# Performance work log

Measured on AMD Instinct MI355X. Metric: run time of the kernel, lower is better.

Reference implementation:

```python
import jax, jax.numpy as jnp
import numpy as np
from jax import lax

V, E, H, L, T, B = 50000, 512, 1024, 2, 512, 64


def _lstm_layer(x_seq, h0, c0, W_ih, W_hh):
    # x_seq: [T, B, D_in]; W_ih: [4H, D_in]; W_hh: [4H, H]
    x_proj = jnp.einsum('tbd,gd->tbg', x_seq, W_ih)  # precompute input projection

    def step(carry, xp):
        h, c = carry
        gates = xp + h @ W_hh.T  # [B, 4H], PyTorch gate order i,f,g,o
        i, f, g, o = jnp.split(gates, 4, axis=-1)
        i = jax.nn.sigmoid(i)
        f = jax.nn.sigmoid(f)
        g = jnp.tanh(g)
        o = jax.nn.sigmoid(o)
        c = f * c + i * g
        h = o * jnp.tanh(c)
        return (h, c), h

    (hT, cT), ys = lax.scan(step, (h0, c0), x_proj)
    return ys, hT, cT


def setup_inputs() -> dict:
    key = jax.random.key(0)
    ks = jax.random.split(key, 8)
    inputs = jax.random.randint(ks[0], (T, B), 0, V)
    h0 = jnp.zeros((L, B, H), jnp.float32)
    c0 = jnp.zeros((L, B, H), jnp.float32)
    emb = jax.random.uniform(ks[1], (V, E), jnp.float32, -0.1, 0.1)
    s_ih0 = 1.0 / np.sqrt(H)
    W_ih0 = jax.random.uniform(ks[2], (4 * H, E), jnp.float32, -s_ih0, s_ih0)
    W_hh0 = jax.random.uniform(ks[3], (4 * H, H), jnp.float32, -s_ih0, s_ih0)
    W_ih1 = jax.random.uniform(ks[4], (4 * H, H), jnp.float32, -s_ih0, s_ih0)
    W_hh1 = jax.random.uniform(ks[5], (4 * H, H), jnp.float32, -s_ih0, s_ih0)
    dec_W = jax.random.uniform(ks[6], (1, H), jnp.float32, -0.1, 0.1)
    dec_b = jnp.zeros((1,), jnp.float32)
    return {"inputs": inputs, "h0": h0, "c0": c0, "emb": emb,
            "W_ih0": W_ih0, "W_hh0": W_hh0, "W_ih1": W_ih1, "W_hh1": W_hh1,
            "dec_W": dec_W, "dec_b": dec_b}


def reference(inputs, h0, c0, emb, W_ih0, W_hh0, W_ih1, W_hh1, dec_W, dec_b):
    x = emb[inputs]                                      # [T, B, E]
    y0, h1, c1 = _lstm_layer(x, h0[0], c0[0], W_ih0, W_hh0)   # [T, B, H]
    # dropout between layers is inference-disabled (eval mode)
    y1, h2, c2 = _lstm_layer(y0, h0[1], c0[1], W_ih1, W_hh1)  # [T, B, H]
    pooled = jnp.mean(y1, axis=0)                        # [B, H] (squeeze is a no-op)
    decoded = pooled @ dec_W.T + dec_b                   # [B, 1]
    hn = jnp.stack([h1, h2])
    cn = jnp.stack([c1, c2])
    return decoded, hn, cn
```

## Files before the change

kernel.cpp:

```cpp
#include <hip/hip_runtime.h>

#define TT 512
#define BB 64
#define HH 1024
#define EE 512
#define VV 50000
#define BBHH (BB*HH)
#define BPL 128
#define NBLK 256

typedef __attribute__((ext_vector_type(8))) short bf16x8;
typedef __attribute__((ext_vector_type(4))) float f32x4;

__device__ inline unsigned short f2b(float f){
  unsigned int u; __builtin_memcpy(&u, &f, 4);
  unsigned int r = (u + 0x7FFFu + ((u >> 16) & 1u)) >> 16;
  return (unsigned short)r;
}
__device__ inline float sigmoidf_(float x){ return 1.0f / (1.0f + __expf(-x)); }
__device__ inline float tanhf_(float x){ float e = __expf(2.0f * x); return 1.0f - 2.0f / (e + 1.0f); }

__device__ inline bf16x8 pack8(float4 a, float4 b){
  bf16x8 r;
  r[0] = (short)f2b(a.x); r[1] = (short)f2b(a.y); r[2] = (short)f2b(a.z); r[3] = (short)f2b(a.w);
  r[4] = (short)f2b(b.x); r[5] = (short)f2b(b.y); r[6] = (short)f2b(b.z); r[7] = (short)f2b(b.w);
  return r;
}

__global__ void cast_f2b(const float* __restrict__ src, unsigned short* __restrict__ dst, long n){
  long i = ((long)blockIdx.x * blockDim.x + threadIdx.x) * 4;
  long stride = (long)gridDim.x * blockDim.x * 4;
  for (; i + 3 < n; i += stride){
    float4 v = *reinterpret_cast<const float4*>(src + i);
    ushort4 r;
    r.x = f2b(v.x); r.y = f2b(v.y); r.z = f2b(v.z); r.w = f2b(v.w);
    *reinterpret_cast<ushort4*>(dst + i) = r;
  }
}

__global__ void init_h(const float* __restrict__ h0,
                       unsigned short* __restrict__ h0ic, unsigned short* __restrict__ h1ic){
  int i = blockIdx.x * blockDim.x + threadIdx.x;
  int b = i >> 10, j = i & (HH - 1);
  int d = (((j >> 3) * BB) + b) * 8 + (j & 7);
  h0ic[d] = f2b(h0[i]);
  h1ic[d] = f2b(h0[BBHH + i]);
}

__device__ __forceinline__ void wait_layer(const unsigned* __restrict__ f, unsigned e, int lane){
  unsigned a = __hip_atomic_load(f + lane,      __ATOMIC_RELAXED, __HIP_MEMORY_SCOPE_AGENT);
  unsigned b = __hip_atomic_load(f + 64 + lane, __ATOMIC_RELAXED, __HIP_MEMORY_SCOPE_AGENT);
  while (!__all(a >= e && b >= e)){
    __builtin_amdgcn_s_sleep(8);
    a = __hip_atomic_load(f + lane,      __ATOMIC_RELAXED, __HIP_MEMORY_SCOPE_AGENT);
    b = __hip_atomic_load(f + 64 + lane, __ATOMIC_RELAXED, __HIP_MEMORY_SCOPE_AGENT);
  }
}

__device__ __forceinline__ void publish(unsigned* __restrict__ f, int bid_l, unsigned e){
  asm volatile("s_waitcnt vmcnt(0)" ::: "memory");
  __syncthreads();
  if (threadIdx.x == 0)
    __hip_atomic_store(f + bid_l, e, __ATOMIC_RELAXED, __HIP_MEMORY_SCOPE_AGENT);
}

#define LIDX(m, s) ((((m) * 16 + (s)) * 64 + lane) * 4)

#define CBASE ((wid * 32 + hi) * (BB * 8) + l16 * 8)

__device__ void run_l0(
    int bid_l, int lane, int wid, int l16, int hi, int kq,
    const int* __restrict__ inputs, const float* __restrict__ c0,
    const unsigned short* __restrict__ emb_bf,
    const float* __restrict__ Wih0, const float* __restrict__ Whh0,
    const unsigned short* __restrict__ h0ic,
    unsigned short* __restrict__ hist0,
    float* __restrict__ hn, float* __restrict__ cn,
    unsigned* __restrict__ flags0, float* lds)
{
  const int j0 = bid_l * 8;
  const int bown = wid * 16 + l16;
  const int cbase = CBASE;

  bf16x8 wx[2][4], wh[2][8];
  #pragma unroll
  for (int m = 0; m < 2; ++m){
    const int g = l16 & 3;
    const int u = 2 * (l16 >> 2) + m;
    const float* rx = Wih0 + (size_t)(g * HH + j0 + u) * EE;
    const float* rh = Whh0 + (size_t)(g * HH + j0 + u) * HH;
    #pragma unroll
    for (int kk = 0; kk < 4; ++kk){
      int k0 = wid * 128 + kk * 32 + kq;
      wx[m][kk] = pack8(*reinterpret_cast<const float4*>(rx + k0),
                        *reinterpret_cast<const float4*>(rx + k0 + 4));
    }
    #pragma unroll
    for (int kk = 0; kk < 8; ++kk){
      int k0 = wid * 256 + kk * 32 + kq;
      wh[m][kk] = pack8(*reinterpret_cast<const float4*>(rh + k0),
                        *reinterpret_cast<const float4*>(rh + k0 + 4));
    }
  }

  float cs[2];
  #pragma unroll
  for (int m = 0; m < 2; ++m)
    cs[m] = c0[(size_t)bown * HH + j0 + 2 * hi + m];

  for (int t = 0; t < TT; ++t){
    f32x4 acc[2][4];
    #pragma unroll
    for (int m = 0; m < 2; ++m)
      #pragma unroll
      for (int nt = 0; nt < 4; ++nt)
        acc[m][nt] = (f32x4){0.f,0.f,0.f,0.f};

    {
      const unsigned short* xr[4];
      #pragma unroll
      for (int nt = 0; nt < 4; ++nt)
        xr[nt] = emb_bf + (size_t)inputs[t * BB + nt * 16 + l16] * EE;
      #pragma unroll
      for (int kk = 0; kk < 4; ++kk){
        const int kb = wid * 128 + kk * 32 + kq;
        #pragma unroll
        for (int nt = 0; nt < 4; ++nt){
          bf16x8 bf = *reinterpret_cast<const bf16x8*>(xr[nt] + kb);
          acc[0][nt] = __builtin_amdgcn_mfma_f32_16x16x32_bf16(wx[0][kk], bf, acc[0][nt], 0, 0, 0);
          acc[1][nt] = __builtin_amdgcn_mfma_f32_16x16x32_bf16(wx[1][kk], bf, acc[1][nt], 0, 0, 0);
        }
      }
    }

    if (t > 0) wait_layer(flags0, (unsigned)t, lane);

    {
      const unsigned short* hs = (t == 0) ? h0ic : hist0 + (size_t)(t - 1) * BBHH;
      #pragma unroll
      for (int kk = 0; kk < 8; ++kk){
        #pragma unroll
        for (int nt = 0; nt < 4; ++nt){
          bf16x8 bf = *reinterpret_cast<const bf16x8*>(hs + cbase + kk * 2048 + nt * 128);
          acc[0][nt] = __builtin_amdgcn_mfma_f32_16x16x32_bf16(wh[0][kk], bf, acc[0][nt], 0, 0, 0);
          acc[1][nt] = __builtin_amdgcn_mfma_f32_16x16x32_bf16(wh[1][kk], bf, acc[1][nt], 0, 0, 0);
        }
      }
    }

    #pragma unroll
    for (int m = 0; m < 2; ++m)
      #pragma unroll
      for (int nt = 0; nt < 4; ++nt)
        *reinterpret_cast<f32x4*>(&lds[LIDX(m, wid * 4 + nt)]) = acc[m][nt];
    __syncthreads();
    f32x4 s[2];
    #pragma unroll
    for (int m = 0; m < 2; ++m){
      s[m] = (f32x4){0.f,0.f,0.f,0.f};
      #pragma unroll
      for (int w = 0; w < 4; ++w)
        s[m] += *reinterpret_cast<f32x4*>(&lds[LIDX(m, w * 4 + wid)]);
    }

    float hv[2];
    #pragma unroll
    for (int m = 0; m < 2; ++m){
      float gi = sigmoidf_(s[m][0]), gf = sigmoidf_(s[m][1]);
      float gg = tanhf_(s[m][2]),    go = sigmoidf_(s[m][3]);
      cs[m] = gf * cs[m] + gi * gg;
      hv[m] = go * tanhf_(cs[m]);
    }
    unsigned w = (unsigned)f2b(hv[0]) | ((unsigned)f2b(hv[1]) << 16);
    __hip_atomic_store(reinterpret_cast<unsigned*>(hist0 + (size_t)t * BBHH + (size_t)(bid_l * BB + bown) * 8 + 2 * hi),
                       w, __ATOMIC_RELAXED, __HIP_MEMORY_SCOPE_AGENT);
    if (t == TT - 1){
      size_t o = (size_t)bown * HH + j0 + 2 * hi;
      *reinterpret_cast<float2*>(hn + o) = make_float2(hv[0], hv[1]);
      *reinterpret_cast<float2*>(cn + o) = make_float2(cs[0], cs[1]);
    }

    publish(flags0, bid_l, (unsigned)(t + 1));
  }
}

__device__ void run_l1(
    int bid_l, int lane, int wid, int l16, int hi, int kq,
    const float* __restrict__ c0,
    const float* __restrict__ Wih1, const float* __restrict__ Whh1,
    const unsigned short* __restrict__ h1ic,
    const unsigned short* __restrict__ hist0, unsigned short* __restrict__ hist1,
    const float* __restrict__ decW, const float* __restrict__ decb,
    float* __restrict__ dec_out, float* __restrict__ hn, float* __restrict__ cn,
    unsigned* __restrict__ flags0, unsigned* __restrict__ flags1, float* lds)
{
  const int j0 = bid_l * 8;
  const int bown = wid * 16 + l16;
  const int cbase = CBASE;

  bf16x8 wx[2][8], wh[2][8];
  #pragma unroll
  for (int m = 0; m < 2; ++m){
    const int g = l16 & 3;
    const int u = 2 * (l16 >> 2) + m;
    const float* rx = Wih1 + (size_t)(g * HH + j0 + u) * HH;
    const float* rh = Whh1 + (size_t)(g * HH + j0 + u) * HH;
    #pragma unroll
    for (int kk = 0; kk < 8; ++kk){
      int k0 = wid * 256 + kk * 32 + kq;
      wx[m][kk] = pack8(*reinterpret_cast<const float4*>(rx + k0),
                        *reinterpret_cast<const float4*>(rx + k0 + 4));
      wh[m][kk] = pack8(*reinterpret_cast<const float4*>(rh + k0),
                        *reinterpret_cast<const float4*>(rh + k0 + 4));
    }
  }

  float cs[2];
  #pragma unroll
  for (int m = 0; m < 2; ++m)
    cs[m] = c0[(size_t)BBHH + (size_t)bown * HH + j0 + 2 * hi + m];
  float pooldec = 0.0f;
  const float dwv0 = decW[j0 + 2 * hi], dwv1 = decW[j0 + 2 * hi + 1];

  for (int t = 0; t < TT; ++t){
    f32x4 acc[2][4];
    #pragma unroll
    for (int m = 0; m < 2; ++m)
      #pragma unroll
      for (int nt = 0; nt < 4; ++nt)
        acc[m][nt] = (f32x4){0.f,0.f,0.f,0.f};

    if (t > 0) wait_layer(flags1, (unsigned)t, lane);
    {
      const unsigned short* hs = (t == 0) ? h1ic : hist1 + (size_t)(t - 1) * BBHH;
      #pragma unroll
      for (int kk = 0; kk < 8; ++kk){
        #pragma unroll
        for (int nt = 0; nt < 4; ++nt){
          bf16x8 bf = *reinterpret_cast<const bf16x8*>(hs + cbase + kk * 2048 + nt * 128);
          acc[0][nt] = __builtin_amdgcn_mfma_f32_16x16x32_bf16(wh[0][kk], bf, acc[0][nt], 0, 0, 0);
          acc[1][nt] = __builtin_amdgcn_mfma_f32_16x16x32_bf16(wh[1][kk], bf, acc[1][nt], 0, 0, 0);
        }
      }
    }

    wait_layer(flags0, (unsigned)(t + 1), lane);
    {
      const unsigned short* xs = hist0 + (size_t)t * BBHH;
      #pragma unroll
      for (int kk = 0; kk < 8; ++kk){
        #pragma unroll
        for (int nt = 0; nt < 4; ++nt){
          bf16x8 bf = *reinterpret_cast<const bf16x8*>(xs + cbase + kk * 2048 + nt * 128);
          acc[0][nt] = __builtin_amdgcn_mfma_f32_16x16x32_bf16(wx[0][kk], bf, acc[0][nt], 0, 0, 0);
          acc[1][nt] = __builtin_amdgcn_mfma_f32_16x16x32_bf16(wx[1][kk], bf, acc[1][nt], 0, 0, 0);
        }
      }
    }

    #pragma unroll
    for (int m = 0; m < 2; ++m)
      #pragma unroll
      for (int nt = 0; nt < 4; ++nt)
        *reinterpret_cast<f32x4*>(&lds[LIDX(m, wid * 4 + nt)]) = acc[m][nt];
    __syncthreads();
    f32x4 s[2];
    #pragma unroll
    for (int m = 0; m < 2; ++m){
      s[m] = (f32x4){0.f,0.f,0.f,0.f};
      #pragma unroll
      for (int w = 0; w < 4; ++w)
        s[m] += *reinterpret_cast<f32x4*>(&lds[LIDX(m, w * 4 + wid)]);
    }

    float hv[2];
    #pragma unroll
    for (int m = 0; m < 2; ++m){
      float gi = sigmoidf_(s[m][0]), gf = sigmoidf_(s[m][1]);
      float gg = tanhf_(s[m][2]),    go = sigmoidf_(s[m][3]);
      cs[m] = gf * cs[m] + gi * gg;
      hv[m] = go * tanhf_(cs[m]);
    }
    unsigned w = (unsigned)f2b(hv[0]) | ((unsigned)f2b(hv[1]) << 16);
    __hip_atomic_store(reinterpret_cast<unsigned*>(hist1 + (size_t)t * BBHH + (size_t)(bid_l * BB + bown) * 8 + 2 * hi),
                       w, __ATOMIC_RELAXED, __HIP_MEMORY_SCOPE_AGENT);
    pooldec += hv[0] * dwv0 + hv[1] * dwv1;
    if (t == TT - 1){
      size_t o = (size_t)BBHH + (size_t)bown * HH + j0 + 2 * hi;
      *reinterpret_cast<float2*>(hn + o) = make_float2(hv[0], hv[1]);
      *reinterpret_cast<float2*>(cn + o) = make_float2(cs[0], cs[1]);
    }

    publish(flags1, bid_l, (unsigned)(t + 1));
  }

  pooldec += __shfl_xor(pooldec, 16);
  pooldec += __shfl_xor(pooldec, 32);
  if (hi == 0){
    float contrib = pooldec * (1.0f / (float)TT);
    if (bid_l == 0) contrib += decb[0];
    atomicAdd(&dec_out[bown], contrib);
  }
}

__global__ __launch_bounds__(256, 1) void lstm_persist(
    const int* __restrict__ inputs, const float* __restrict__ c0,
    const unsigned short* __restrict__ emb_bf,
    const float* __restrict__ Wih0, const float* __restrict__ Whh0,
    const float* __restrict__ Wih1, const float* __restrict__ Whh1,
    const unsigned short* __restrict__ h0ic, const unsigned short* __restrict__ h1ic,
    unsigned short* __restrict__ hist0, unsigned short* __restrict__ hist1,
    const float* __restrict__ decW, const float* __restrict__ decb,
    float* __restrict__ dec_out, float* __restrict__ hn, float* __restrict__ cn,
    unsigned* __restrict__ flags)
{
  __shared__ float lds[2 * 16 * 64 * 4];
  const int tid  = threadIdx.x;
  const int lane = tid & 63;
  const int wid  = tid >> 6;
  const int l16  = lane & 15;
  const int hi   = lane >> 4;
  const int kq   = hi << 3;
  unsigned* flags0 = flags;
  unsigned* flags1 = flags + 128;

  int bid = blockIdx.x;
  if (bid < BPL){
    run_l0(bid, lane, wid, l16, hi, kq, inputs, c0, emb_bf, Wih0, Whh0,
           h0ic, hist0, hn, cn, flags0, lds);
  } else {
    run_l1(bid - BPL, lane, wid, l16, hi, kq, c0, Wih1, Whh1,
           h1ic, hist0, hist1, decW, decb, dec_out, hn, cn, flags0, flags1, lds);
  }
}

extern "C" void kernel_launch(void* const* d_in, const int* in_sizes, int n_in,
                              void* d_out, int out_size, void* d_ws, size_t ws_size,
                              hipStream_t stream){
  const int*   inputs = (const int*)d_in[0];
  const float* h0     = (const float*)d_in[1];
  const float* c0     = (const float*)d_in[2];
  const float* emb    = (const float*)d_in[3];
  const float* Wih0   = (const float*)d_in[4];
  const float* Whh0   = (const float*)d_in[5];
  const float* Wih1   = (const float*)d_in[6];
  const float* Whh1   = (const float*)d_in[7];
  const float* decW   = (const float*)d_in[8];
  const float* decb   = (const float*)d_in[9];

  char* ws = (char*)d_ws;
  size_t off = 0;
  auto alloc = [&](size_t bytes) -> void* {
    void* p = ws + off;
    off += (bytes + 255) & ~(size_t)255;
    return p;
  };
  unsigned short* emb_bf = (unsigned short*)alloc((size_t)VV * EE * 2);
  unsigned short* hist0  = (unsigned short*)alloc((size_t)TT * BBHH * 2);
  unsigned short* hist1  = (unsigned short*)alloc((size_t)TT * BBHH * 2);
  unsigned short* h0ic   = (unsigned short*)alloc((size_t)BBHH * 2);
  unsigned short* h1ic   = (unsigned short*)alloc((size_t)BBHH * 2);
  unsigned int*   flags  = (unsigned int*)alloc((size_t)256 * 4);

  float* out = (float*)d_out;
  float* hn  = out + BB;
  float* cn  = out + BB + 2 * BBHH;

  hipMemsetAsync(flags, 0, 256 * 4, stream);
  hipMemsetAsync(out, 0, BB * 4, stream);

  cast_f2b<<<2048, 256, 0, stream>>>(emb, emb_bf, (long)VV * EE);
  init_h<<<BBHH / 256, 256, 0, stream>>>(h0, h0ic, h1ic);

  lstm_persist<<<NBLK, 256, 0, stream>>>(inputs, c0, emb_bf,
                                         Wih0, Whh0, Wih1, Whh1,
                                         h0ic, h1ic, hist0, hist1,
                                         decW, decb, out, hn, cn, flags);
}
```

Baseline: 4.286 ms.

## Halve persistent block count with 512-thread blocks and defer flag publish

Each layer now runs on 64 blocks of 512 threads instead of 128 blocks of 256, and each block owns 16 hidden units split into two halves of 8 waves. This halves the number of flags each block polls per timestep (one 64-lane load instead of two). The flag publish for step t is moved to just before waiting on step t's dependencies, so the drain is overlapped with the input-projection MFMAs. In layer 1 the input projection from layer 0 is now computed before waiting on its own recurrence. The cost is larger blocks, a bigger LDS reduction buffer, and a later publish that may delay peers.

```diff
diff --git a/kernel.cpp b/kernel.cpp
--- a/kernel.cpp
+++ b/kernel.cpp
@@ -6,40 +6,43 @@
 #define EE 512
 #define VV 50000
 #define BBHH (BB*HH)
-#define BPL 128
-#define NBLK 256
+#define NBL 64
+#define NBLK 128
 
 typedef __attribute__((ext_vector_type(8))) short bf16x8;
 typedef __attribute__((ext_vector_type(4))) float f32x4;
-
-__device__ inline unsigned short f2b(float f){
-  unsigned int u; __builtin_memcpy(&u, &f, 4);
-  unsigned int r = (u + 0x7FFFu + ((u >> 16) & 1u)) >> 16;
-  return (unsigned short)r;
+typedef unsigned short us;
+
+#define MFMA(a,b,c) __builtin_amdgcn_mfma_f32_16x16x32_bf16((a),(b),(c),0,0,0)
+#define LDG(p) __hip_atomic_load((p), __ATOMIC_RELAXED, __HIP_MEMORY_SCOPE_AGENT)
+#define ZI(uh,ksw,m,nt,ln) ((((((uh)*4+(ksw))*2+(m))*4+(nt))*64+(ln))*4)
+
+__device__ inline us f2b(float f){
+  unsigned u; __builtin_memcpy(&u, &f, 4);
+  return (us)((u + 0x7FFFu + ((u >> 16) & 1u)) >> 16);
 }
 __device__ inline float sigmoidf_(float x){ return 1.0f / (1.0f + __expf(-x)); }
 __device__ inline float tanhf_(float x){ float e = __expf(2.0f * x); return 1.0f - 2.0f / (e + 1.0f); }
 
 __device__ inline bf16x8 pack8(float4 a, float4 b){
   bf16x8 r;
-  r[0] = (short)f2b(a.x); r[1] = (short)f2b(a.y); r[2] = (short)f2b(a.z); r[3] = (short)f2b(a.w);
-  r[4] = (short)f2b(b.x); r[5] = (short)f2b(b.y); r[6] = (short)f2b(b.z); r[7] = (short)f2b(b.w);
+  r[0]=(short)f2b(a.x); r[1]=(short)f2b(a.y); r[2]=(short)f2b(a.z); r[3]=(short)f2b(a.w);
+  r[4]=(short)f2b(b.x); r[5]=(short)f2b(b.y); r[6]=(short)f2b(b.z); r[7]=(short)f2b(b.w);
   return r;
 }
 
-__global__ void cast_f2b(const float* __restrict__ src, unsigned short* __restrict__ dst, long n){
+__global__ void cast_f2b(const float* __restrict__ src, us* __restrict__ dst, long n){
   long i = ((long)blockIdx.x * blockDim.x + threadIdx.x) * 4;
   long stride = (long)gridDim.x * blockDim.x * 4;
   for (; i + 3 < n; i += stride){
     float4 v = *reinterpret_cast<const float4*>(src + i);
-    ushort4 r;
-    r.x = f2b(v.x); r.y = f2b(v.y); r.z = f2b(v.z); r.w = f2b(v.w);
+    ushort4 r; r.x=f2b(v.x); r.y=f2b(v.y); r.z=f2b(v.z); r.w=f2b(v.w);
     *reinterpret_cast<ushort4*>(dst + i) = r;
   }
 }
 
 __global__ void init_h(const float* __restrict__ h0,
-                       unsigned short* __restrict__ h0ic, unsigned short* __restrict__ h1ic){
+                       us* __restrict__ h0ic, us* __restrict__ h1ic){
   int i = blockIdx.x * blockDim.x + threadIdx.x;
   int b = i >> 10, j = i & (HH - 1);
   int d = (((j >> 3) * BB) + b) * 8 + (j & 7);
@@ -47,103 +50,95 @@
   h1ic[d] = f2b(h0[BBHH + i]);
 }
 
-__device__ __forceinline__ void wait_layer(const unsigned* __restrict__ f, unsigned e, int lane){
-  unsigned a = __hip_atomic_load(f + lane,      __ATOMIC_RELAXED, __HIP_MEMORY_SCOPE_AGENT);
-  unsigned b = __hip_atomic_load(f + 64 + lane, __ATOMIC_RELAXED, __HIP_MEMORY_SCOPE_AGENT);
-  while (!__all(a >= e && b >= e)){
-    __builtin_amdgcn_s_sleep(8);
-    a = __hip_atomic_load(f + lane,      __ATOMIC_RELAXED, __HIP_MEMORY_SCOPE_AGENT);
-    b = __hip_atomic_load(f + 64 + lane, __ATOMIC_RELAXED, __HIP_MEMORY_SCOPE_AGENT);
-  }
-}
-
-__device__ __forceinline__ void publish(unsigned* __restrict__ f, int bid_l, unsigned e){
+__device__ __forceinline__ void wait64(const unsigned* __restrict__ f, unsigned e, int lane){
+  unsigned a = LDG(f + lane);
+  while (!__all((int)(a >= e))){
+    __builtin_amdgcn_s_sleep(4);
+    a = LDG(f + lane);
+  }
+}
+__device__ __forceinline__ void drain_flag(unsigned* __restrict__ fl, unsigned e){
   asm volatile("s_waitcnt vmcnt(0)" ::: "memory");
   __syncthreads();
   if (threadIdx.x == 0)
-    __hip_atomic_store(f + bid_l, e, __ATOMIC_RELAXED, __HIP_MEMORY_SCOPE_AGENT);
-}
-
-#define LIDX(m, s) ((((m) * 16 + (s)) * 64 + lane) * 4)
-
-#define CBASE ((wid * 32 + hi) * (BB * 8) + l16 * 8)
-
-__device__ void run_l0(
-    int bid_l, int lane, int wid, int l16, int hi, int kq,
+    __hip_atomic_store(fl, e, __ATOMIC_RELAXED, __HIP_MEMORY_SCOPE_AGENT);
+}
+
+__device__ void run_l0(int bid_l,
     const int* __restrict__ inputs, const float* __restrict__ c0,
-    const unsigned short* __restrict__ emb_bf,
+    const us* __restrict__ emb_bf,
     const float* __restrict__ Wih0, const float* __restrict__ Whh0,
-    const unsigned short* __restrict__ h0ic,
-    unsigned short* __restrict__ hist0,
+    const us* __restrict__ h0ic, us* __restrict__ hist0,
     float* __restrict__ hn, float* __restrict__ cn,
-    unsigned* __restrict__ flags0, float* lds)
+    unsigned* __restrict__ flags0, float* zone)
 {
-  const int j0 = bid_l * 8;
-  const int bown = wid * 16 + l16;
-  const int cbase = CBASE;
+  const int tid = threadIdx.x, lane = tid & 63, wid = tid >> 6;
+  const int l16 = lane & 15, hi = lane >> 4, kq = hi << 3;
+  const int ks = wid & 3, uh = wid >> 2;
+  const int j0 = bid_l * 16;
 
   bf16x8 wx[2][4], wh[2][8];
   #pragma unroll
   for (int m = 0; m < 2; ++m){
     const int g = l16 & 3;
-    const int u = 2 * (l16 >> 2) + m;
-    const float* rx = Wih0 + (size_t)(g * HH + j0 + u) * EE;
-    const float* rh = Whh0 + (size_t)(g * HH + j0 + u) * HH;
+    const int ug = j0 + uh * 8 + 2 * (l16 >> 2) + m;
+    const float* rx = Wih0 + (size_t)(g * HH + ug) * EE;
+    const float* rh = Whh0 + (size_t)(g * HH + ug) * HH;
     #pragma unroll
     for (int kk = 0; kk < 4; ++kk){
-      int k0 = wid * 128 + kk * 32 + kq;
-      wx[m][kk] = pack8(*reinterpret_cast<const float4*>(rx + k0),
-                        *reinterpret_cast<const float4*>(rx + k0 + 4));
+      int k0 = ks * 128 + kk * 32 + kq;
+      wx[m][kk] = pack8(*(const float4*)(rx + k0), *(const float4*)(rx + k0 + 4));
     }
     #pragma unroll
     for (int kk = 0; kk < 8; ++kk){
-      int k0 = wid * 256 + kk * 32 + kq;
-      wh[m][kk] = pack8(*reinterpret_cast<const float4*>(rh + k0),
-                        *reinterpret_cast<const float4*>(rh + k0 + 4));
-    }
-  }
-
+      int k0 = ks * 256 + kk * 32 + kq;
+      wh[m][kk] = pack8(*(const float4*)(rh + k0), *(const float4*)(rh + k0 + 4));
+    }
+  }
+
+  const int b_own = ks * 16 + l16;
+  const int u0    = j0 + uh * 8 + 2 * hi;
   float cs[2];
   #pragma unroll
-  for (int m = 0; m < 2; ++m)
-    cs[m] = c0[(size_t)bown * HH + j0 + 2 * hi + m];
+  for (int m = 0; m < 2; ++m) cs[m] = c0[(size_t)b_own * HH + u0 + m];
 
   for (int t = 0; t < TT; ++t){
     f32x4 acc[2][4];
     #pragma unroll
     for (int m = 0; m < 2; ++m)
       #pragma unroll
-      for (int nt = 0; nt < 4; ++nt)
-        acc[m][nt] = (f32x4){0.f,0.f,0.f,0.f};
+      for (int nt = 0; nt < 4; ++nt) acc[m][nt] = (f32x4){0.f,0.f,0.f,0.f};
 
     {
-      const unsigned short* xr[4];
+      const us* xr[4];
       #pragma unroll
       for (int nt = 0; nt < 4; ++nt)
         xr[nt] = emb_bf + (size_t)inputs[t * BB + nt * 16 + l16] * EE;
       #pragma unroll
       for (int kk = 0; kk < 4; ++kk){
-        const int kb = wid * 128 + kk * 32 + kq;
+        const int kb = ks * 128 + kk * 32 + kq;
         #pragma unroll
         for (int nt = 0; nt < 4; ++nt){
-          bf16x8 bf = *reinterpret_cast<const bf16x8*>(xr[nt] + kb);
-          acc[0][nt] = __builtin_amdgcn_mfma_f32_16x16x32_bf16(wx[0][kk], bf, acc[0][nt], 0, 0, 0);
-          acc[1][nt] = __builtin_amdgcn_mfma_f32_16x16x32_bf16(wx[1][kk], bf, acc[1][nt], 0, 0, 0);
+          bf16x8 bf = *(const bf16x8*)(xr[nt] + kb);
+          acc[0][nt] = MFMA(wx[0][kk], bf, acc[0][nt]);
+          acc[1][nt] = MFMA(wx[1][kk], bf, acc[1][nt]);
         }
       }
     }
 
-    if (t > 0) wait_layer(flags0, (unsigned)t, lane);
+    if (t > 0) drain_flag(flags0 + bid_l, (unsigned)t);
+    if (t > 0) wait64(flags0, (unsigned)t, lane);
 
     {
-      const unsigned short* hs = (t == 0) ? h0ic : hist0 + (size_t)(t - 1) * BBHH;
+      const us* hs = (t == 0) ? h0ic : hist0 + (size_t)(t - 1) * BBHH;
       #pragma unroll
       for (int kk = 0; kk < 8; ++kk){
+        const us* p = hs + (size_t)(ks * 32 + kk * 4 + hi) * (BB * 8);
         #pragma unroll
         for (int nt = 0; nt < 4; ++nt){
-          bf16x8 bf = *reinterpret_cast<const bf16x8*>(hs + cbase + kk * 2048 + nt * 128);
-          acc[0][nt] = __builtin_amdgcn_mfma_f32_16x16x32_bf16(wh[0][kk], bf, acc[0][nt], 0, 0, 0);
-          acc[1][nt] = __builtin_amdgcn_mfma_f32_16x16x32_bf16(wh[1][kk], bf, acc[1][nt], 0, 0, 0);
+          bf16x8 bf = *(const bf16x8*)(p + (nt * 16 + l16) * 8);
+          acc[0][nt] = MFMA(wh[0][kk], bf, acc[0][nt]);
+          acc[1][nt] = MFMA(wh[1][kk], bf, acc[1][nt]);
         }
       }
     }
@@ -152,15 +147,15 @@
     for (int m = 0; m < 2; ++m)
       #pragma unroll
       for (int nt = 0; nt < 4; ++nt)
-        *reinterpret_cast<f32x4*>(&lds[LIDX(m, wid * 4 + nt)]) = acc[m][nt];
+        *(f32x4*)&zone[ZI(uh, ks, m, nt, lane)] = acc[m][nt];
     __syncthreads();
     f32x4 s[2];
     #pragma unroll
     for (int m = 0; m < 2; ++m){
       s[m] = (f32x4){0.f,0.f,0.f,0.f};
       #pragma unroll
-      for (int w = 0; w < 4; ++w)
-        s[m] += *reinterpret_cast<f32x4*>(&lds[LIDX(m, w * 4 + wid)]);
+      for (int kr = 0; kr < 4; ++kr)
+        s[m] += *(f32x4*)&zone[ZI(uh, kr, m, ks, lane)];
     }
 
     float hv[2];
@@ -172,88 +167,89 @@
       hv[m] = go * tanhf_(cs[m]);
     }
     unsigned w = (unsigned)f2b(hv[0]) | ((unsigned)f2b(hv[1]) << 16);
-    __hip_atomic_store(reinterpret_cast<unsigned*>(hist0 + (size_t)t * BBHH + (size_t)(bid_l * BB + bown) * 8 + 2 * hi),
+    __hip_atomic_store((unsigned*)(hist0 + (size_t)t * BBHH +
+                        ((size_t)((2 * bid_l + uh) * BB + b_own)) * 8 + 2 * hi),
                        w, __ATOMIC_RELAXED, __HIP_MEMORY_SCOPE_AGENT);
     if (t == TT - 1){
-      size_t o = (size_t)bown * HH + j0 + 2 * hi;
+      size_t o = (size_t)b_own * HH + u0;
       *reinterpret_cast<float2*>(hn + o) = make_float2(hv[0], hv[1]);
       *reinterpret_cast<float2*>(cn + o) = make_float2(cs[0], cs[1]);
     }
-
-    publish(flags0, bid_l, (unsigned)(t + 1));
-  }
-}
-
-__device__ void run_l1(
-    int bid_l, int lane, int wid, int l16, int hi, int kq,
+  }
+  drain_flag(flags0 + bid_l, (unsigned)TT);
+}
+
+__device__ void run_l1(int bid_l,
     const float* __restrict__ c0,
     const float* __restrict__ Wih1, const float* __restrict__ Whh1,
-    const unsigned short* __restrict__ h1ic,
-    const unsigned short* __restrict__ hist0, unsigned short* __restrict__ hist1,
+    const us* __restrict__ h1ic, const us* __restrict__ hist0, us* __restrict__ hist1,
     const float* __restrict__ decW, const float* __restrict__ decb,
     float* __restrict__ dec_out, float* __restrict__ hn, float* __restrict__ cn,
-    unsigned* __restrict__ flags0, unsigned* __restrict__ flags1, float* lds)
+    unsigned* __restrict__ flags0, unsigned* __restrict__ flags1, float* zone)
 {
-  const int j0 = bid_l * 8;
-  const int bown = wid * 16 + l16;
-  const int cbase = CBASE;
+  const int tid = threadIdx.x, lane = tid & 63, wid = tid >> 6;
+  const int l16 = lane & 15, hi = lane >> 4, kq = hi << 3;
+  const int ks = wid & 3, uh = wid >> 2;
+  const int j0 = bid_l * 16;
 
   bf16x8 wx[2][8], wh[2][8];
   #pragma unroll
   for (int m = 0; m < 2; ++m){
     const int g = l16 & 3;
-    const int u = 2 * (l16 >> 2) + m;
-    const float* rx = Wih1 + (size_t)(g * HH + j0 + u) * HH;
-    const float* rh = Whh1 + (size_t)(g * HH + j0 + u) * HH;
+    const int ug = j0 + uh * 8 + 2 * (l16 >> 2) + m;
+    const float* rx = Wih1 + (size_t)(g * HH + ug) * HH;
+    const float* rh = Whh1 + (size_t)(g * HH + ug) * HH;
     #pragma unroll
     for (int kk = 0; kk < 8; ++kk){
-      int k0 = wid * 256 + kk * 32 + kq;
-      wx[m][kk] = pack8(*reinterpret_cast<const float4*>(rx + k0),
-                        *reinterpret_cast<const float4*>(rx + k0 + 4));
-      wh[m][kk] = pack8(*reinterpret_cast<const float4*>(rh + k0),
-                        *reinterpret_cast<const float4*>(rh + k0 + 4));
-    }
-  }
-
+      int k0 = ks * 256 + kk * 32 + kq;
+      wx[m][kk] = pack8(*(const float4*)(rx + k0), *(const float4*)(rx + k0 + 4));
+      wh[m][kk] = pack8(*(const float4*)(rh + k0), *(const float4*)(rh + k0 + 4));
+    }
+  }
+
+  const int b_own = ks * 16 + l16;
+  const int u0    = j0 + uh * 8 + 2 * hi;
   float cs[2];
   #pragma unroll
-  for (int m = 0; m < 2; ++m)
-    cs[m] = c0[(size_t)BBHH + (size_t)bown * HH + j0 + 2 * hi + m];
-  float pooldec = 0.0f;
-  const float dwv0 = decW[j0 + 2 * hi], dwv1 = decW[j0 + 2 * hi + 1];
+  for (int m = 0; m < 2; ++m) cs[m] = c0[(size_t)BBHH + (size_t)b_own * HH + u0 + m];
+  float pooldec = 0.f;
+  const float dw0 = decW[u0], dw1 = decW[u0 + 1];
 
   for (int t = 0; t < TT; ++t){
     f32x4 acc[2][4];
     #pragma unroll
     for (int m = 0; m < 2; ++m)
       #pragma unroll
-      for (int nt = 0; nt < 4; ++nt)
-        acc[m][nt] = (f32x4){0.f,0.f,0.f,0.f};
-
-    if (t > 0) wait_layer(flags1, (unsigned)t, lane);
+      for (int nt = 0; nt < 4; ++nt) acc[m][nt] = (f32x4){0.f,0.f,0.f,0.f};
+
+    wait64(flags0, (unsigned)(t + 1), lane);
     {
-      const unsigned short* hs = (t == 0) ? h1ic : hist1 + (size_t)(t - 1) * BBHH;
+      const us* xs = hist0 + (size_t)t * BBHH;
       #pragma unroll
       for (int kk = 0; kk < 8; ++kk){
+        const us* p = xs + (size_t)(ks * 32 + kk * 4 + hi) * (BB * 8);
         #pragma unroll
         for (int nt = 0; nt < 4; ++nt){
-          bf16x8 bf = *reinterpret_cast<const bf16x8*>(hs + cbase + kk * 2048 + nt * 128);
-          acc[0][nt] = __builtin_amdgcn_mfma_f32_16x16x32_bf16(wh[0][kk], bf, acc[0][nt], 0, 0, 0);
-          acc[1][nt] = __builtin_amdgcn_mfma_f32_16x16x32_bf16(wh[1][kk], bf, acc[1][nt], 0, 0, 0);
+          bf16x8 bf = *(const bf16x8*)(p + (nt * 16 + l16) * 8);
+          acc[0][nt] = MFMA(wx[0][kk], bf, acc[0][nt]);
+          acc[1][nt] = MFMA(wx[1][kk], bf, acc[1][nt]);
         }
       }
     }
 
-    wait_layer(flags0, (unsigned)(t + 1), lane);
+    if (t > 0) drain_flag(flags1 + bid_l, (unsigned)t);
+    if (t > 0) wait64(flags1, (unsigned)t, lane);
+
     {
-      const unsigned short* xs = hist0 + (size_t)t * BBHH;
+      const us* hs = (t == 0) ? h1ic : hist1 + (size_t)(t - 1) * BBHH;
       #pragma unroll
       for (int kk = 0; kk < 8; ++kk){
+        const us* p = hs + (size_t)(ks * 32 + kk * 4 + hi) * (BB * 8);
         #pragma unroll
         for (int nt = 0; nt < 4; ++nt){
-          bf16x8 bf = *reinterpret_cast<const bf16x8*>(xs + cbase + kk * 2048 + nt * 128);
-          acc[0][nt] = __builtin_amdgcn_mfma_f32_16x16x32_bf16(wx[0][kk], bf, acc[0][nt], 0, 0, 0);
-          acc[1][nt] = __builtin_amdgcn_mfma_f32_16x16x32_bf16(wx[1][kk], bf, acc[1][nt], 0, 0, 0);
+          bf16x8 bf = *(const bf16x8*)(p + (nt * 16 + l16) * 8);
+          acc[0][nt] = MFMA(wh[0][kk], bf, acc[0][nt]);
+          acc[1][nt] = MFMA(wh[1][kk], bf, acc[1][nt]);
         }
       }
     }
@@ -262,15 +258,15 @@
     for (int m = 0; m < 2; ++m)
       #pragma unroll
       for (int nt = 0; nt < 4; ++nt)
-        *reinterpret_cast<f32x4*>(&lds[LIDX(m, wid * 4 + nt)]) = acc[m][nt];
+        *(f32x4*)&zone[ZI(uh, ks, m, nt, lane)] = acc[m][nt];
     __syncthreads();
     f32x4 s[2];
     #pragma unroll
     for (int m = 0; m < 2; ++m){
       s[m] = (f32x4){0.f,0.f,0.f,0.f};
       #pragma unroll
-      for (int w = 0; w < 4; ++w)
-        s[m] += *reinterpret_cast<f32x4*>(&lds[LIDX(m, w * 4 + wid)]);
+      for (int kr = 0; kr < 4; ++kr)
+        s[m] += *(f32x4*)&zone[ZI(uh, kr, m, ks, lane)];
     }
 
     float hv[2];
@@ -282,55 +278,47 @@
       hv[m] = go * tanhf_(cs[m]);
     }
     unsigned w = (unsigned)f2b(hv[0]) | ((unsigned)f2b(hv[1]) << 16);
-    __hip_atomic_store(reinterpret_cast<unsigned*>(hist1 + (size_t)t * BBHH + (size_t)(bid_l * BB + bown) * 8 + 2 * hi),
+    __hip_atomic_store((unsigned*)(hist1 + (size_t)t * BBHH +
+                        ((size_t)((2 * bid_l + uh) * BB + b_own)) * 8 + 2 * hi),
                        w, __ATOMIC_RELAXED, __HIP_MEMORY_SCOPE_AGENT);
-    pooldec += hv[0] * dwv0 + hv[1] * dwv1;
+    pooldec += hv[0] * dw0 + hv[1] * dw1;
     if (t == TT - 1){
-      size_t o = (size_t)BBHH + (size_t)bown * HH + j0 + 2 * hi;
+      size_t o = (size_t)BBHH + (size_t)b_own * HH + u0;
       *reinterpret_cast<float2*>(hn + o) = make_float2(hv[0], hv[1]);
       *reinterpret_cast<float2*>(cn + o) = make_float2(cs[0], cs[1]);
     }
-
-    publish(flags1, bid_l, (unsigned)(t + 1));
   }
 
   pooldec += __shfl_xor(pooldec, 16);
   pooldec += __shfl_xor(pooldec, 32);
-  if (hi == 0){
+  if (lane < 16){
     float contrib = pooldec * (1.0f / (float)TT);
-    if (bid_l == 0) contrib += decb[0];
-    atomicAdd(&dec_out[bown], contrib);
-  }
-}
-
-__global__ __launch_bounds__(256, 1) void lstm_persist(
+    if (bid_l == 0 && uh == 0) contrib += decb[0];
+    atomicAdd(&dec_out[ks * 16 + lane], contrib);
+  }
+}
+
+__global__ __launch_bounds__(512, 2) void lstm_persist(
     const int* __restrict__ inputs, const float* __restrict__ c0,
-    const unsigned short* __restrict__ emb_bf,
+    const us* __restrict__ emb_bf,
     const float* __restrict__ Wih0, const float* __restrict__ Whh0,
     const float* __restrict__ Wih1, const float* __restrict__ Whh1,
-    const unsigned short* __restrict__ h0ic, const unsigned short* __restrict__ h1ic,
-    unsigned short* __restrict__ hist0, unsigned short* __restrict__ hist1,
+    const us* __restrict__ h0ic, const us* __restrict__ h1ic,
+    us* __restrict__ hist0, us* __restrict__ hist1,
     const float* __restrict__ decW, const float* __restrict__ decb,
     float* __restrict__ dec_out, float* __restrict__ hn, float* __restrict__ cn,
     unsigned* __restrict__ flags)
 {
-  __shared__ float lds[2 * 16 * 64 * 4];
-  const int tid  = threadIdx.x;
-  const int lane = tid & 63;
-  const int wid  = tid >> 6;
-  const int l16  = lane & 15;
-  const int hi   = lane >> 4;
-  const int kq   = hi << 3;
+  __shared__ float zone[2 * 4 * 2 * 4 * 64 * 4];
   unsigned* flags0 = flags;
-  unsigned* flags1 = flags + 128;
-
+  unsigned* flags1 = flags + 64;
   int bid = blockIdx.x;
-  if (bid < BPL){
-    run_l0(bid, lane, wid, l16, hi, kq, inputs, c0, emb_bf, Wih0, Whh0,
-           h0ic, hist0, hn, cn, flags0, lds);
+  if (bid < NBL){
+    run_l0(bid, inputs, c0, emb_bf, Wih0, Whh0, h0ic, hist0,
+           hn, cn, flags0, zone);
   } else {
-    run_l1(bid - BPL, lane, wid, l16, hi, kq, c0, Wih1, Whh1,
-           h1ic, hist0, hist1, decW, decb, dec_out, hn, cn, flags0, flags1, lds);
+    run_l1(bid - NBL, c0, Wih1, Whh1, h1ic, hist0, hist1, decW, decb,
+           dec_out, hn, cn, flags0, flags1, zone);
   }
 }
 
@@ -355,24 +343,24 @@
     off += (bytes + 255) & ~(size_t)255;
     return p;
   };
-  unsigned short* emb_bf = (unsigned short*)alloc((size_t)VV * EE * 2);
-  unsigned short* hist0  = (unsigned short*)alloc((size_t)TT * BBHH * 2);
-  unsigned short* hist1  = (unsigned short*)alloc((size_t)TT * BBHH * 2);
-  unsigned short* h0ic   = (unsigned short*)alloc((size_t)BBHH * 2);
-  unsigned short* h1ic   = (unsigned short*)alloc((size_t)BBHH * 2);
-  unsigned int*   flags  = (unsigned int*)alloc((size_t)256 * 4);
+  us* emb_bf = (us*)alloc((size_t)VV * EE * 2);
+  us* hist0  = (us*)alloc((size_t)TT * BBHH * 2);
+  us* hist1  = (us*)alloc((size_t)TT * BBHH * 2);
+  us* h0ic   = (us*)alloc((size_t)BBHH * 2);
+  us* h1ic   = (us*)alloc((size_t)BBHH * 2);
+  unsigned* flags = (unsigned*)alloc((size_t)128 * 4);
 
   float* out = (float*)d_out;
   float* hn  = out + BB;
   float* cn  = out + BB + 2 * BBHH;
 
-  hipMemsetAsync(flags, 0, 256 * 4, stream);
+  hipMemsetAsync(flags, 0, 128 * 4, stream);
   hipMemsetAsync(out, 0, BB * 4, stream);
 
   cast_f2b<<<2048, 256, 0, stream>>>(emb, emb_bf, (long)VV * EE);
   init_h<<<BBHH / 256, 256, 0, stream>>>(h0, h0ic, h1ic);
 
-  lstm_persist<<<NBLK, 256, 0, stream>>>(inputs, c0, emb_bf,
+  lstm_persist<<<NBLK, 512, 0, stream>>>(inputs, c0, emb_bf,
                                          Wih0, Whh0, Wih1, Whh1,
                                          h0ic, h1ic, hist0, hist1,
                                          decW, decb, out, hn, cn, flags);
```

Result: slower. 6.050 ms (+41.2%).

## Defer flag publish past input projection and reorder layer-1 waits

Applied to the files above, without the earlier changes.

Each step's completion flag is now drained and published just before the recurrent wait, not at the end of the step. This lets the store drain overlap the input-projection MFMAs for the next step. Layer 1 now handles the layer-0 input term first and its own recurrent term second, so the wait on its own h happens later. The spin-wait sleep is shortened from 8 to 1 to react faster, at the cost of more polling traffic on the flag lines.

```diff
diff --git a/kernel.cpp b/kernel.cpp
--- a/kernel.cpp
+++ b/kernel.cpp
@@ -11,35 +11,37 @@
 
 typedef __attribute__((ext_vector_type(8))) short bf16x8;
 typedef __attribute__((ext_vector_type(4))) float f32x4;
-
-__device__ inline unsigned short f2b(float f){
-  unsigned int u; __builtin_memcpy(&u, &f, 4);
-  unsigned int r = (u + 0x7FFFu + ((u >> 16) & 1u)) >> 16;
-  return (unsigned short)r;
+typedef unsigned short us;
+
+#define MFMA(a,b,c) __builtin_amdgcn_mfma_f32_16x16x32_bf16((a),(b),(c),0,0,0)
+#define LDG(p) __hip_atomic_load((p), __ATOMIC_RELAXED, __HIP_MEMORY_SCOPE_AGENT)
+
+__device__ inline us f2b(float f){
+  unsigned u; __builtin_memcpy(&u, &f, 4);
+  return (us)((u + 0x7FFFu + ((u >> 16) & 1u)) >> 16);
 }
 __device__ inline float sigmoidf_(float x){ return 1.0f / (1.0f + __expf(-x)); }
 __device__ inline float tanhf_(float x){ float e = __expf(2.0f * x); return 1.0f - 2.0f / (e + 1.0f); }
 
 __device__ inline bf16x8 pack8(float4 a, float4 b){
   bf16x8 r;
-  r[0] = (short)f2b(a.x); r[1] = (short)f2b(a.y); r[2] = (short)f2b(a.z); r[3] = (short)f2b(a.w);
-  r[4] = (short)f2b(b.x); r[5] = (short)f2b(b.y); r[6] = (short)f2b(b.z); r[7] = (short)f2b(b.w);
+  r[0]=(short)f2b(a.x); r[1]=(short)f2b(a.y); r[2]=(short)f2b(a.z); r[3]=(short)f2b(a.w);
+  r[4]=(short)f2b(b.x); r[5]=(short)f2b(b.y); r[6]=(short)f2b(b.z); r[7]=(short)f2b(b.w);
   return r;
 }
 
-__global__ void cast_f2b(const float* __restrict__ src, unsigned short* __restrict__ dst, long n){
+__global__ void cast_f2b(const float* __restrict__ src, us* __restrict__ dst, long n){
   long i = ((long)blockIdx.x * blockDim.x + threadIdx.x) * 4;
   long stride = (long)gridDim.x * blockDim.x * 4;
   for (; i + 3 < n; i += stride){
     float4 v = *reinterpret_cast<const float4*>(src + i);
-    ushort4 r;
-    r.x = f2b(v.x); r.y = f2b(v.y); r.z = f2b(v.z); r.w = f2b(v.w);
+    ushort4 r; r.x=f2b(v.x); r.y=f2b(v.y); r.z=f2b(v.z); r.w=f2b(v.w);
     *reinterpret_cast<ushort4*>(dst + i) = r;
   }
 }
 
 __global__ void init_h(const float* __restrict__ h0,
-                       unsigned short* __restrict__ h0ic, unsigned short* __restrict__ h1ic){
+                       us* __restrict__ h0ic, us* __restrict__ h1ic){
   int i = blockIdx.x * blockDim.x + threadIdx.x;
   int b = i >> 10, j = i & (HH - 1);
   int d = (((j >> 3) * BB) + b) * 8 + (j & 7);
@@ -47,21 +49,19 @@
   h1ic[d] = f2b(h0[BBHH + i]);
 }
 
-__device__ __forceinline__ void wait_layer(const unsigned* __restrict__ f, unsigned e, int lane){
-  unsigned a = __hip_atomic_load(f + lane,      __ATOMIC_RELAXED, __HIP_MEMORY_SCOPE_AGENT);
-  unsigned b = __hip_atomic_load(f + 64 + lane, __ATOMIC_RELAXED, __HIP_MEMORY_SCOPE_AGENT);
-  while (!__all(a >= e && b >= e)){
-    __builtin_amdgcn_s_sleep(8);
-    a = __hip_atomic_load(f + lane,      __ATOMIC_RELAXED, __HIP_MEMORY_SCOPE_AGENT);
-    b = __hip_atomic_load(f + 64 + lane, __ATOMIC_RELAXED, __HIP_MEMORY_SCOPE_AGENT);
-  }
-}
-
-__device__ __forceinline__ void publish(unsigned* __restrict__ f, int bid_l, unsigned e){
+__device__ __forceinline__ void wait128(const unsigned* __restrict__ f, unsigned e, int lane){
+  unsigned a = LDG(f + lane), b = LDG(f + 64 + lane);
+  while (!__all((int)(a >= e && b >= e))){
+    __builtin_amdgcn_s_sleep(1);
+    a = LDG(f + lane); b = LDG(f + 64 + lane);
+  }
+}
+
+__device__ __forceinline__ void drain_flag(unsigned* __restrict__ fl, unsigned e){
   asm volatile("s_waitcnt vmcnt(0)" ::: "memory");
   __syncthreads();
   if (threadIdx.x == 0)
-    __hip_atomic_store(f + bid_l, e, __ATOMIC_RELAXED, __HIP_MEMORY_SCOPE_AGENT);
+    __hip_atomic_store(fl, e, __ATOMIC_RELAXED, __HIP_MEMORY_SCOPE_AGENT);
 }
 
 #define LIDX(m, s) ((((m) * 16 + (s)) * 64 + lane) * 4)
@@ -71,10 +71,10 @@
 __device__ void run_l0(
     int bid_l, int lane, int wid, int l16, int hi, int kq,
     const int* __restrict__ inputs, const float* __restrict__ c0,
-    const unsigned short* __restrict__ emb_bf,
+    const us* __restrict__ emb_bf,
     const float* __restrict__ Wih0, const float* __restrict__ Whh0,
-    const unsigned short* __restrict__ h0ic,
-    unsigned short* __restrict__ hist0,
+    const us* __restrict__ h0ic,
+    us* __restrict__ hist0,
     float* __restrict__ hn, float* __restrict__ cn,
     unsigned* __restrict__ flags0, float* lds)
 {
@@ -117,7 +117,7 @@
         acc[m][nt] = (f32x4){0.f,0.f,0.f,0.f};
 
     {
-      const unsigned short* xr[4];
+      const us* xr[4];
       #pragma unroll
       for (int nt = 0; nt < 4; ++nt)
         xr[nt] = emb_bf + (size_t)inputs[t * BB + nt * 16 + l16] * EE;
@@ -127,23 +127,26 @@
         #pragma unroll
         for (int nt = 0; nt < 4; ++nt){
           bf16x8 bf = *reinterpret_cast<const bf16x8*>(xr[nt] + kb);
-          acc[0][nt] = __builtin_amdgcn_mfma_f32_16x16x32_bf16(wx[0][kk], bf, acc[0][nt], 0, 0, 0);
-          acc[1][nt] = __builtin_amdgcn_mfma_f32_16x16x32_bf16(wx[1][kk], bf, acc[1][nt], 0, 0, 0);
+          acc[0][nt] = MFMA(wx[0][kk], bf, acc[0][nt]);
+          acc[1][nt] = MFMA(wx[1][kk], bf, acc[1][nt]);
         }
       }
     }
 
-    if (t > 0) wait_layer(flags0, (unsigned)t, lane);
+    if (t > 0){
+      drain_flag(flags0 + bid_l, (unsigned)t);
+      wait128(flags0, (unsigned)t, lane);
+    }
 
     {
-      const unsigned short* hs = (t == 0) ? h0ic : hist0 + (size_t)(t - 1) * BBHH;
+      const us* hs = (t == 0) ? h0ic : hist0 + (size_t)(t - 1) * BBHH;
       #pragma unroll
       for (int kk = 0; kk < 8; ++kk){
         #pragma unroll
         for (int nt = 0; nt < 4; ++nt){
           bf16x8 bf = *reinterpret_cast<const bf16x8*>(hs + cbase + kk * 2048 + nt * 128);
-          acc[0][nt] = __builtin_amdgcn_mfma_f32_16x16x32_bf16(wh[0][kk], bf, acc[0][nt], 0, 0, 0);
-          acc[1][nt] = __builtin_amdgcn_mfma_f32_16x16x32_bf16(wh[1][kk], bf, acc[1][nt], 0, 0, 0);
+          acc[0][nt] = MFMA(wh[0][kk], bf, acc[0][nt]);
+          acc[1][nt] = MFMA(wh[1][kk], bf, acc[1][nt]);
         }
       }
     }
@@ -179,17 +182,16 @@
       *reinterpret_cast<float2*>(hn + o) = make_float2(hv[0], hv[1]);
       *reinterpret_cast<float2*>(cn + o) = make_float2(cs[0], cs[1]);
     }
-
-    publish(flags0, bid_l, (unsigned)(t + 1));
-  }
+  }
+  drain_flag(flags0 + bid_l, (unsigned)TT);
 }
 
 __device__ void run_l1(
     int bid_l, int lane, int wid, int l16, int hi, int kq,
     const float* __restrict__ c0,
     const float* __restrict__ Wih1, const float* __restrict__ Whh1,
-    const unsigned short* __restrict__ h1ic,
-    const unsigned short* __restrict__ hist0, unsigned short* __restrict__ hist1,
+    const us* __restrict__ h1ic,
+    const us* __restrict__ hist0, us* __restrict__ hist1,
     const float* __restrict__ decW, const float* __restrict__ decb,
     float* __restrict__ dec_out, float* __restrict__ hn, float* __restrict__ cn,
     unsigned* __restrict__ flags0, unsigned* __restrict__ flags1, float* lds)
@@ -230,30 +232,33 @@
       for (int nt = 0; nt < 4; ++nt)
         acc[m][nt] = (f32x4){0.f,0.f,0.f,0.f};
 
-    if (t > 0) wait_layer(flags1, (unsigned)t, lane);
+    wait128(flags0, (unsigned)(t + 1), lane);
     {
-      const unsigned short* hs = (t == 0) ? h1ic : hist1 + (size_t)(t - 1) * BBHH;
+      const us* xs = hist0 + (size_t)t * BBHH;
+      #pragma unroll
+      for (int kk = 0; kk < 8; ++kk){
+        #pragma unroll
+        for (int nt = 0; nt < 4; ++nt){
+          bf16x8 bf = *reinterpret_cast<const bf16x8*>(xs + cbase + kk * 2048 + nt * 128);
+          acc[0][nt] = MFMA(wx[0][kk], bf, acc[0][nt]);
+          acc[1][nt] = MFMA(wx[1][kk], bf, acc[1][nt]);
+        }
+      }
+    }
+
+    if (t > 0){
+      drain_flag(flags1 + bid_l, (unsigned)t);
+      wait128(flags1, (unsigned)t, lane);
+    }
+    {
+      const us* hs = (t == 0) ? h1ic : hist1 + (size_t)(t - 1) * BBHH;
       #pragma unroll
       for (int kk = 0; kk < 8; ++kk){
         #pragma unroll
         for (int nt = 0; nt < 4; ++nt){
           bf16x8 bf = *reinterpret_cast<const bf16x8*>(hs + cbase + kk * 2048 + nt * 128);
-          acc[0][nt] = __builtin_amdgcn_mfma_f32_16x16x32_bf16(wh[0][kk], bf, acc[0][nt], 0, 0, 0);
-          acc[1][nt] = __builtin_amdgcn_mfma_f32_16x16x32_bf16(wh[1][kk], bf, acc[1][nt], 0, 0, 0);
-        }
-      }
-    }
-
-    wait_layer(flags0, (unsigned)(t + 1), lane);
-    {
-      const unsigned short* xs = hist0 + (size_t)t * BBHH;
-      #pragma unroll
-      for (int kk = 0; kk < 8; ++kk){
-        #pragma unroll
-        for (int nt = 0; nt < 4; ++nt){
-          bf16x8 bf = *reinterpret_cast<const bf16x8*>(xs + cbase + kk * 2048 + nt * 128);
-          acc[0][nt] = __builtin_amdgcn_mfma_f32_16x16x32_bf16(wx[0][kk], bf, acc[0][nt], 0, 0, 0);
-          acc[1][nt] = __builtin_amdgcn_mfma_f32_16x16x32_bf16(wx[1][kk], bf, acc[1][nt], 0, 0, 0);
+          acc[0][nt] = MFMA(wh[0][kk], bf, acc[0][nt]);
+          acc[1][nt] = MFMA(wh[1][kk], bf, acc[1][nt]);
         }
       }
     }
@@ -290,8 +295,6 @@
       *reinterpret_cast<float2*>(hn + o) = make_float2(hv[0], hv[1]);
       *reinterpret_cast<float2*>(cn + o) = make_float2(cs[0], cs[1]);
     }
-
-    publish(flags1, bid_l, (unsigned)(t + 1));
   }
 
   pooldec += __shfl_xor(pooldec, 16);
@@ -305,11 +308,11 @@
 
 __global__ __launch_bounds__(256, 1) void lstm_persist(
     const int* __restrict__ inputs, const float* __restrict__ c0,
-    const unsigned short* __restrict__ emb_bf,
+    const us* __restrict__ emb_bf,
     const float* __restrict__ Wih0, const float* __restrict__ Whh0,
     const float* __restrict__ Wih1, const float* __restrict__ Whh1,
-    const unsigned short* __restrict__ h0ic, const unsigned short* __restrict__ h1ic,
-    unsigned short* __restrict__ hist0, unsigned short* __restrict__ hist1,
+    const us* __restrict__ h0ic, const us* __restrict__ h1ic,
+    us* __restrict__ hist0, us* __restrict__ hist1,
     const float* __restrict__ decW, const float* __restrict__ decb,
     float* __restrict__ dec_out, float* __restrict__ hn, float* __restrict__ cn,
     unsigned* __restrict__ flags)
@@ -355,12 +358,12 @@
     off += (bytes + 255) & ~(size_t)255;
     return p;
   };
-  unsigned short* emb_bf = (unsigned short*)alloc((size_t)VV * EE * 2);
-  unsigned short* hist0  = (unsigned short*)alloc((size_t)TT * BBHH * 2);
-  unsigned short* hist1  = (unsigned short*)alloc((size_t)TT * BBHH * 2);
-  unsigned short* h0ic   = (unsigned short*)alloc((size_t)BBHH * 2);
-  unsigned short* h1ic   = (unsigned short*)alloc((size_t)BBHH * 2);
-  unsigned int*   flags  = (unsigned int*)alloc((size_t)256 * 4);
+  us* emb_bf = (us*)alloc((size_t)VV * EE * 2);
+  us* hist0  = (us*)alloc((size_t)TT * BBHH * 2);
+  us* hist1  = (us*)alloc((size_t)TT * BBHH * 2);
+  us* h0ic   = (us*)alloc((size_t)BBHH * 2);
+  us* h1ic   = (us*)alloc((size_t)BBHH * 2);
+  unsigned* flags = (unsigned*)alloc((size_t)256 * 4);
 
   float* out = (float*)d_out;
   float* hn  = out + BB;
```

Measured after the change: 6.120 ms. 1.43x slower.
